# Optimization experiments

Hardware: AMD Instinct MI355X
Metric: run time of the kernel (lower is better)

## Reference

```python
import jax, jax.numpy as jnp
import numpy as np

B, H, W, C = 8, 128, 128, 192
WS, SS, HEADS = 8, 4, 6
NW = (H // WS) * (W // WS)
N = WS * WS

def _rel_pos_index(ws):
    coords = np.stack(np.meshgrid(np.arange(ws), np.arange(ws), indexing='ij')).reshape(2, -1)
    rel = (coords[:, :, None] - coords[:, None, :]).transpose(1, 2, 0)
    rel[:, :, 0] += ws - 1
    rel[:, :, 1] += ws - 1
    rel[:, :, 0] *= 2 * ws - 1
    return rel.sum(-1)  # (N, N) int

REL_IDX = jnp.asarray(_rel_pos_index(WS).reshape(-1))

def setup_inputs():
    key = jax.random.key(0)
    ks = jax.random.split(key, 8)
    p = lambda k, shp: jax.random.normal(k, shp, jnp.float32) * 0.02
    # exact Swin shift mask for shift=(SS,SS)
    img = np.zeros((1, H, W, 1), np.float32)
    cnt = 0
    for hs in (slice(0, -WS), slice(-WS, -SS), slice(-SS, None)):
        for vs in (slice(0, -WS), slice(-WS, -SS), slice(-SS, None)):
            img[:, hs, vs, :] = cnt; cnt += 1
    mw = img.reshape(1, H // WS, WS, W // WS, WS, 1).transpose(0, 1, 3, 2, 4, 5).reshape(-1, N)
    diff = mw[:, None, :] - mw[:, :, None]
    mask = np.where(diff != 0, -100.0, 0.0).astype(np.float32)
    return dict(
        x=jax.random.normal(ks[0], (B, H, W, C), jnp.float32),
        mask_matrix=jnp.asarray(mask),
        norm1_g=jnp.ones((C,), jnp.float32), norm1_b=jnp.zeros((C,), jnp.float32),
        qkv_w=p(ks[1], (C, 3 * C)), qkv_b=jnp.zeros((3 * C,), jnp.float32),
        rel_bias_table=p(ks[2], ((2 * WS - 1) * (2 * WS - 1), HEADS)),
        proj_w=p(ks[3], (C, C)), proj_b=jnp.zeros((C,), jnp.float32),
        norm2_g=jnp.ones((C,), jnp.float32), norm2_b=jnp.zeros((C,), jnp.float32),
        fc1_w=p(ks[4], (C, 4 * C)), fc1_b=jnp.zeros((4 * C,), jnp.float32),
        fc2_w=p(ks[5], (4 * C, C)), fc2_b=jnp.zeros((C,), jnp.float32),
    )

def _ln(x, g, b):
    m = x.mean(-1, keepdims=True)
    v = x.var(-1, keepdims=True)
    return (x - m) * jax.lax.rsqrt(v + 1e-5) * g + b

def _window_attn(xw, mask, qkv_w, qkv_b, rel_bias_table, proj_w, proj_b):
    Bw = xw.shape[0]
    hd = C // HEADS
    scale = hd ** -0.5
    # ---- spatial window attention ----
    qkv = (xw @ qkv_w + qkv_b).reshape(Bw, N, 3, HEADS, hd).transpose(2, 0, 3, 1, 4)
    q, k, v = qkv[0], qkv[1], qkv[2]  # (Bw, heads, N, hd)
    attn = jnp.einsum('bhnd,bhmd->bhnm', q, k) * scale
    bias = rel_bias_table[REL_IDX].reshape(N, N, HEADS).transpose(2, 0, 1)
    attn = attn + bias[None]
    attn = attn.reshape(Bw // NW, NW, HEADS, N, N) + mask[None, :, None]
    attn = jax.nn.softmax(attn.reshape(Bw, HEADS, N, N), axis=-1)
    x_spatial = jnp.einsum('bhnm,bhmd->bhnd', attn, v).transpose(0, 2, 1, 3).reshape(Bw, N, C)
    # ---- Fourier-domain attention branch ----
    x2d = xw.reshape(Bw, WS, WS, C)
    xf = jnp.fft.rfftn(x2d, axes=(1, 2), norm='ortho')  # (Bw, WS, WS//2+1, C) complex
    Hf, Wf = xf.shape[1], xf.shape[2]
    Nf = Hf * Wf
    def _qkv(r):  # shared qkv linear applied to real/imag parts (bias in both)
        return (r.reshape(Bw, Nf, C) @ qkv_w + qkv_b).reshape(Bw, Nf, 3, HEADS, hd).transpose(2, 0, 3, 1, 4)
    qr, qi = _qkv(xf.real), _qkv(xf.imag)
    qf = jax.lax.complex(qr[0], qi[0])
    kf = jax.lax.complex(qr[1], qi[1])
    vf = jax.lax.complex(qr[2], qi[2])
    attn_f = jnp.einsum('bhnd,bhmd->bhnm', qf, kf) * scale  # plain transpose, no conj (matches torch)
    attn_mag = jax.nn.softmax(jnp.abs(attn_f), axis=-1)
    xf_res = jnp.einsum('bhnm,bhmd->bhnd', attn_mag.astype(jnp.complex64), vf)
    xf_res = xf_res.transpose(0, 2, 1, 3).reshape(Bw, Hf, Wf, C)
    x_four = jnp.fft.irfftn(xf_res, s=(WS, WS), axes=(1, 2), norm='ortho').reshape(Bw, N, C)
    return (x_spatial + x_four) @ proj_w + proj_b

def reference(x, mask_matrix, norm1_g, norm1_b, qkv_w, qkv_b, rel_bias_table,
              proj_w, proj_b, norm2_g, norm2_b, fc1_w, fc1_b, fc2_w, fc2_b):
    shortcut = x
    xn = _ln(x, norm1_g, norm1_b)
    # shift (H,W divisible by WS so no padding needed)
    xs = jnp.roll(xn, (-SS, -SS), axis=(1, 2))
    # window partition -> (B*nW, N, C)
    xw = xs.reshape(B, H // WS, WS, W // WS, WS, C).transpose(0, 1, 3, 2, 4, 5).reshape(-1, N, C)
    aw = _window_attn(xw, mask_matrix, qkv_w, qkv_b, rel_bias_table, proj_w, proj_b)
    # window reverse + unshift
    xs = aw.reshape(B, H // WS, W // WS, WS, WS, C).transpose(0, 1, 3, 2, 4, 5).reshape(B, H, W, C)
    xo = jnp.roll(xs, (SS, SS), axis=(1, 2))
    x1 = shortcut + xo
    y = _ln(x1, norm2_g, norm2_b)
    y = jax.nn.gelu(y @ fc1_w + fc1_b, approximate=False) @ fc2_w + fc2_b
    return x1 + y
```

## Files before the change

### kernel.cpp

```cpp
#include <hip/hip_runtime.h>
#include <hip/hip_bf16.h>
#include <math.h>

#define SSH 4
#define SCALE 0.17677669529663687f

typedef __bf16 bf16x8 __attribute__((ext_vector_type(8)));
typedef __bf16 bf16x4 __attribute__((ext_vector_type(4)));
typedef unsigned short ushort8 __attribute__((ext_vector_type(8)));
typedef float  f32x4  __attribute__((ext_vector_type(4)));

static __device__ __forceinline__ f32x4 mfma16(bf16x8 a, bf16x8 b, f32x4 c){
    return __builtin_amdgcn_mfma_f32_16x16x32_bf16(a, b, c, 0, 0, 0);
}
#define MFMA16(a,b,c) mfma16((a),(b),(c))

static __device__ __forceinline__ bf16x8 ldfrag(const __bf16* p){
    return *reinterpret_cast<const bf16x8*>(p);
}
static __device__ __forceinline__ f32x4 zero4(){
    f32x4 z; z[0]=0.f; z[1]=0.f; z[2]=0.f; z[3]=0.f; return z;
}
static __device__ __forceinline__ float gelu_fast(float x){
    float u = x*(0.7978845608f + 0.0356774081f*x*x);
    return __fdividef(x, 1.f + __expf(-2.f*u));
}

__global__ __launch_bounds__(256) void k_prep(const float* __restrict__ qkvw,
        const float* __restrict__ projw, const float* __restrict__ fc1w,
        const float* __restrict__ fc2w, __bf16* __restrict__ Wq,
        __bf16* __restrict__ Wp, __bf16* __restrict__ W1, __bf16* __restrict__ W2,
        __bf16* __restrict__ Fre, __bf16* __restrict__ Fim,
        __bf16* __restrict__ Ci,  __bf16* __restrict__ nSi){
    int i = blockIdx.x*256 + threadIdx.x;
    if (i < 110592){ int n = i/192, k = i - n*192; Wq[i] = (__bf16)qkvw[k*576 + n]; }
    if (i < 36864) { int n = i/192, k = i - n*192; Wp[i] = (__bf16)projw[k*192 + n]; }
    if (i < 147456){ int n = i/192, k = i - n*192; W1[i] = (__bf16)fc1w[k*768 + n]; }
    if (i < 147456){ int n = i/768, k = i - n*768; W2[i] = (__bf16)fc2w[k*192 + n]; }
    if (i < 3072){
        int n = i>>6, p = i&63;
        float vr = 0.f, vi = 0.f;
        if (n < 40){
            int u = n/5, v = n - u*5, r = p>>3, c = p&7;
            int k = (u*r + v*c)&7;
            float ang = (float)k * 0.78539816339744831f;
            vr = cosf(ang)*0.125f; vi = -sinf(ang)*0.125f;
        }
        Fre[i] = (__bf16)vr; Fim[i] = (__bf16)vi;
    }
    if (i < 4096){
        int p = i>>6, n = i&63;
        float vc = 0.f, vs = 0.f;
        if (n < 40){
            int u = n/5, v = n - u*5, r = p>>3, c = p&7;
            int k = (u*r + v*c)&7;
            float ang = (float)k * 0.78539816339744831f;
            float wv = (v>=1 && v<=3)? 2.f : 1.f;
            vc = wv*cosf(ang)*0.125f; vs = -wv*sinf(ang)*0.125f;
        }
        Ci[i] = (__bf16)vc; nSi[i] = (__bf16)vs;
    }
}

__global__ __launch_bounds__(256,2) void k_qkv(const float* __restrict__ x,
        const float* __restrict__ n1g, const float* __restrict__ n1b,
        const __bf16* __restrict__ Wqt, const float* __restrict__ qkv_b,
        __bf16* __restrict__ S){
    __shared__ __align__(16) __bf16 xw[64*200];
    __shared__ __align__(16) __bf16 Wt[192*72];
    int tid = threadIdx.x;
    int win = blockIdx.x;
    int bb = win>>8, rem = win&255, wh = rem>>4, wwi = rem&15;
    {
        int tok = tid>>2, part = tid&3;
        int r = tok>>3, c = tok&7;
        int sh = (wh*8 + r + SSH)&127, sw = (wwi*8 + c + SSH)&127;
        const float* srcp = x + (((size_t)(bb*128+sh))*128 + sw)*192 + part*48;
        float v[48];
        #pragma unroll
        for (int i=0;i<12;i++){
            float4 t4 = *reinterpret_cast<const float4*>(srcp + i*4);
            v[i*4]=t4.x; v[i*4+1]=t4.y; v[i*4+2]=t4.z; v[i*4+3]=t4.w;
        }
        float s=0.f, ss=0.f;
        #pragma unroll
        for (int i=0;i<48;i++){ s+=v[i]; ss+=v[i]*v[i]; }
        s  += __shfl_xor(s,1);  s  += __shfl_xor(s,2);
        ss += __shfl_xor(ss,1); ss += __shfl_xor(ss,2);
        float mean = s*(1.f/192.f);
        float rstd = rsqrtf(ss*(1.f/192.f) - mean*mean + 1e-5f);
        #pragma unroll
        for (int i8=0;i8<6;i8++){
            bf16x8 pk;
            #pragma unroll
            for (int j=0;j<8;j++){
                int ch = part*48 + i8*8 + j;
                pk[j] = (__bf16)((v[i8*8+j]-mean)*rstd*n1g[ch] + n1b[ch]);
            }
            *reinterpret_cast<bf16x8*>(&xw[tok*200 + part*48 + i8*8]) = pk;
        }
    }
    int lane = tid&63, w = tid>>6, lr = lane&15, lg = lane>>4;
    ushort8 wreg[6];
    auto ldW = [&](int s, ushort8* wr){
        int nc = s/3, kc = s - nc*3;
        #pragma unroll
        for (int i=0;i<6;i++){
            int e = tid + i*256;
            int j = e>>3, k8 = e&7;
            wr[i] = *reinterpret_cast<const ushort8*>(
                reinterpret_cast<const unsigned short*>(Wqt) + (size_t)(nc*192+j)*192 + kc*64 + k8*8);
        }
    };
    auto stW = [&](ushort8* wr){
        #pragma unroll
        for (int i=0;i<6;i++){
            int e = tid + i*256;
            int j = e>>3, k8 = e&7;
            *reinterpret_cast<ushort8*>(reinterpret_cast<unsigned short*>(Wt) + j*72 + k8*8) = wr[i];
        }
    };
    ldW(0, wreg);
    __syncthreads();
    stW(wreg);
    __syncthreads();
    f32x4 acc[4][3];
    #pragma unroll
    for (int m=0;m<4;m++)
        #pragma unroll
        for (int n=0;n<3;n++) acc[m][n] = zero4();
    for (int s=0; s<9; s++){
        int nc = s/3, kc = s - nc*3;
        if (s<8) ldW(s+1, wreg);
        #pragma unroll
        for (int kk=0; kk<2; kk++){
            int ko = kc*64 + kk*32 + lg*8;
            bf16x8 a[4];
            #pragma unroll
            for (int m=0;m<4;m++) a[m] = ldfrag(&xw[(16*m+lr)*200 + ko]);
            int klo = kk*32 + lg*8;
            bf16x8 bfr[3];
            #pragma unroll
            for (int n=0;n<3;n++) bfr[n] = ldfrag(&Wt[(48*w+16*n+lr)*72 + klo]);
            #pragma unroll
            for (int m=0;m<4;m++)
                #pragma unroll
                for (int n=0;n<3;n++) acc[m][n] = MFMA16(a[m], bfr[n], acc[m][n]);
        }
        if (kc==2){
            #pragma unroll
            for (int n=0;n<3;n++){
                int col = nc*192 + 48*w + 16*n + lr;
                float bias = qkv_b[col];
                #pragma unroll
                for (int m=0;m<4;m++)
                    #pragma unroll
                    for (int r=0;r<4;r++){
                        int row = 16*m + 4*lg + r;
                        S[(size_t)(win*64+row)*576 + col] = (__bf16)(acc[m][n][r] + bias);
                    }
            }
            #pragma unroll
            for (int m=0;m<4;m++)
                #pragma unroll
                for (int n=0;n<3;n++) acc[m][n] = zero4();
        }
        __syncthreads();
        if (s<8) stW(wreg);
        __syncthreads();
    }
}

__global__ __launch_bounds__(256,4) void k_spatial(const __bf16* __restrict__ S,
        const float* __restrict__ relt, const float* __restrict__ mask,
        float* __restrict__ Bbuf){
    __shared__ __align__(16) __bf16 P[64*72];
    __shared__ __align__(16) __bf16 Vt[32*72];
    __shared__ float reltL[1350];
    int tid = threadIdx.x;
    int win = blockIdx.x;
    int widx = win & 255;
    int lane = tid&63, w = tid>>6, lr = lane&15, lg = lane>>4;
    for (int e=tid; e<1350; e+=256) reltL[e] = relt[e];
    float mreg[16];
    int bidx[16];
    #pragma unroll
    for (int nt=0; nt<4; nt++)
        #pragma unroll
        for (int r=0;r<4;r++){
            int row = 16*w + 4*lg + r;
            int col = 16*nt + lr;
            mreg[nt*4+r] = mask[((widx*64 + row)<<6) + col];
            int dr = (row>>3)-(col>>3)+7, dc = (row&7)-(col&7)+7;
            bidx[nt*4+r] = (dr*15+dc)*6;
        }
    const size_t sbase = (size_t)win*64*576;
    const __bf16* Sq = S + sbase;
    const __bf16* Sk = S + sbase + 192;
    const __bf16* Sv = S + sbase + 384;
    for (int h=0; h<6; h++){
        __syncthreads();
        {
            int d = tid&31, pg = tid>>5;
            const __bf16* sp = Sv + (size_t)(pg*8)*576 + h*32 + d;
            bf16x4 v0, v1;
            v0[0]=sp[0];    v0[1]=sp[576];  v0[2]=sp[1152]; v0[3]=sp[1728];
            v1[0]=sp[2304]; v1[1]=sp[2880]; v1[2]=sp[3456]; v1[3]=sp[4032];
            *reinterpret_cast<bf16x4*>(&Vt[d*72 + pg*8])   = v0;
            *reinterpret_cast<bf16x4*>(&Vt[d*72 + pg*8+4]) = v1;
        }
        __syncthreads();
        bf16x8 aq = ldfrag(Sq + (size_t)(16*w+lr)*576 + h*32 + lg*8);
        f32x4 acc[4];
        #pragma unroll
        for (int nt=0;nt<4;nt++){
            bf16x8 bk = ldfrag(Sk + (size_t)(16*nt+lr)*576 + h*32 + lg*8);
            acc[nt] = MFMA16(aq, bk, zero4());
        }
        float p[16];
        #pragma unroll
        for (int r=0;r<4;r++){
            float sc[4];
            #pragma unroll
            for (int nt=0;nt<4;nt++)
                sc[nt] = acc[nt][r]*SCALE + reltL[bidx[nt*4+r] + h] + mreg[nt*4+r];
            float mx = fmaxf(fmaxf(sc[0],sc[1]),fmaxf(sc[2],sc[3]));
            mx = fmaxf(mx, __shfl_xor(mx,1));
            mx = fmaxf(mx, __shfl_xor(mx,2));
            mx = fmaxf(mx, __shfl_xor(mx,4));
            mx = fmaxf(mx, __shfl_xor(mx,8));
            float sum = 0.f;
            #pragma unroll
            for (int nt=0;nt<4;nt++){ sc[nt] = __expf(sc[nt]-mx); sum += sc[nt]; }
            sum += __shfl_xor(sum,1);
            sum += __shfl_xor(sum,2);
            sum += __shfl_xor(sum,4);
            sum += __shfl_xor(sum,8);
            float inv = 1.f/sum;
            #pragma unroll
            for (int nt=0;nt<4;nt++) p[r*4+nt] = sc[nt]*inv;
        }
        #pragma unroll
        for (int r=0;r<4;r++)
            #pragma unroll
            for (int nt=0;nt<4;nt++)
                P[(16*w + 4*lg + r)*72 + 16*nt + lr] = (__bf16)p[r*4+nt];
        #pragma unroll
        for (int dt=0; dt<2; dt++){
            f32x4 o = zero4();
            #pragma unroll
            for (int ks=0; ks<2; ks++)
                o = MFMA16(ldfrag(&P[(16*w+lr)*72 + ks*32 + lg*8]),
                           ldfrag(&Vt[(16*dt+lr)*72 + ks*32 + lg*8]), o);
            #pragma unroll
            for (int r=0;r<4;r++){
                int row = 16*w + 4*lg + r;
                Bbuf[((size_t)win*64 + row)*192 + h*32 + 16*dt + lr] = o[r];
            }
        }
    }
}

__global__ __launch_bounds__(256,3) void k_fattn(const __bf16* __restrict__ S,
        const float* __restrict__ qkv_b,
        const __bf16* __restrict__ Fre_g, const __bf16* __restrict__ Fim_g,
        const __bf16* __restrict__ Ci_g,  const __bf16* __restrict__ nSi_g,
        float* __restrict__ Bbuf){
    __shared__ __align__(16) unsigned char arena[45056];
    __bf16* Gq_r = (__bf16*)(arena);
    __bf16* Gqin = (__bf16*)(arena + 3840);
    __bf16* Gk_r = (__bf16*)(arena + 7680);
    __bf16* Gk_i = (__bf16*)(arena + 11520);
    __bf16* Rt_r = (__bf16*)(arena);
    __bf16* Rt_i = (__bf16*)(arena + 5632);
    __bf16* Gv_r = (__bf16*)(arena + 15360);
    __bf16* Gv_i = (__bf16*)(arena + 20992);
    __bf16* St   = (__bf16*)(arena + 26624);
    float*  Smat = (float*) (arena + 26624);
    __bf16* P    = (__bf16*)(arena + 36608);
    int tid = threadIdx.x;
    int win = blockIdx.x / 6, h = blockIdx.x - win*6;
    int lane = tid&63, w = tid>>6, lr = lane&15, lg = lane>>4;
    bf16x4 z4; z4[0]=z4[1]=z4[2]=z4[3]=(__bf16)0.f;
    {
        int t2 = tid & 127;
        __bf16* A = (tid<128)? Gv_r : Gv_i;
        int row = t2>>2, c4 = (t2&3)*4;
        *reinterpret_cast<bf16x4*>(A + row*88 + 48 + c4) = z4;
    }
    const size_t sbase = (size_t)win*64*576 + h*32;
    for (int m=0;m<3;m++){
        __syncthreads();
        {
            int d = tid&31, pg = tid>>5;
            const __bf16* sp = S + sbase + (size_t)m*192 + (size_t)pg*8*576 + d;
            bf16x4 v0, v1;
            v0[0]=sp[0];      v0[1]=sp[576];    v0[2]=sp[1152];   v0[3]=sp[1728];
            v1[0]=sp[2304];   v1[1]=sp[2880];   v1[2]=sp[3456];   v1[3]=sp[4032];
            *reinterpret_cast<bf16x4*>(&St[d*88 + pg*8])     = v0;
            *reinterpret_cast<bf16x4*>(&St[d*88 + pg*8 + 4]) = v1;
        }
        __syncthreads();
        for (int j=w; j<12; j+=4){
            int term = j/6, r2 = j - term*6;
            if (m<2){
                int mt = r2>>1, nt = r2&1;
                const __bf16* Ag = (term? Fim_g : Fre_g) + (16*mt+lr)*64 + lg*8;
                f32x4 acc = zero4();
                acc = MFMA16(*reinterpret_cast<const bf16x8*>(Ag),
                             ldfrag(&St[(16*nt+lr)*88 + lg*8]), acc);
                acc = MFMA16(*reinterpret_cast<const bf16x8*>(Ag+32),
                             ldfrag(&St[(16*nt+lr)*88 + 32 + lg*8]), acc);
                int d = 16*nt + lr;
                float b = qkv_b[m*192 + h*32 + d];
                __bf16* dst = (m==0)? (term? Gqin : Gq_r) : (term? Gk_i : Gk_r);
                #pragma unroll
                for (int r=0;r<4;r++){
                    int n = 16*mt + 4*lg + r;
                    float val = acc[r] + ((term==0) ? ((n==0)? -7.f*b : b) : b);
                    if (m==0 && term==1) val = -val;
                    dst[n*40 + d] = (__bf16)val;
                }
            } else {
                int mt = r2/3, nt = r2 - mt*3;
                const __bf16* Bg = (term? Fim_g : Fre_g) + (16*nt+lr)*64 + lg*8;
                f32x4 acc = zero4();
                acc = MFMA16(ldfrag(&St[(16*mt+lr)*88 + lg*8]),
                             *reinterpret_cast<const bf16x8*>(Bg), acc);
                acc = MFMA16(ldfrag(&St[(16*mt+lr)*88 + 32 + lg*8]),
                             *reinterpret_cast<const bf16x8*>(Bg+32), acc);
                int n = 16*nt + lr;
                __bf16* dst = term? Gv_i : Gv_r;
                #pragma unroll
                for (int r=0;r<4;r++){
                    int d = 16*mt + 4*lg + r;
                    float b = qkv_b[2*192 + h*32 + d];
                    float val = acc[r] + ((term==0) ? ((n==0)? -7.f*b : b) : b);
                    dst[d*88 + n] = (__bf16)val;
                }
            }
        }
    }
    __syncthreads();
    for (int j=w; j<9; j+=4){
        int mt = j/3, nt = j - mt*3;
        bf16x8 qr = ldfrag(&Gq_r[(16*mt+lr)*40 + lg*8]);
        bf16x8 qi = ldfrag(&Gqin[(16*mt+lr)*40 + lg*8]);
        bf16x8 kr = ldfrag(&Gk_r[(16*nt+lr)*40 + lg*8]);
        bf16x8 ki = ldfrag(&Gk_i[(16*nt+lr)*40 + lg*8]);
        f32x4 sre = MFMA16(qi, ki, zero4());
        sre = MFMA16(qr, kr, sre);
        f32x4 t1 = MFMA16(qr, ki, zero4());
        f32x4 t2 = MFMA16(qi, kr, zero4());
        #pragma unroll
        for (int r=0;r<4;r++){
            float sim = t1[r] - t2[r];
            Smat[(16*mt + 4*lg + r)*52 + 16*nt + lr] =
                SCALE * sqrtf(sre[r]*sre[r] + sim*sim);
        }
    }
    __syncthreads();
    if (tid < 160){
        int row = tid>>2, part = tid&3, e0 = part*10;
        float mx = -1e30f;
        #pragma unroll
        for (int j=0;j<10;j++) mx = fmaxf(mx, Smat[row*52 + e0 + j]);
        mx = fmaxf(mx, __shfl_xor(mx,1));
        mx = fmaxf(mx, __shfl_xor(mx,2));
        float ex[10]; float sum=0.f;
        #pragma unroll
        for (int j=0;j<10;j++){ ex[j] = __expf(Smat[row*52+e0+j]-mx); sum += ex[j]; }
        sum += __shfl_xor(sum,1);
        sum += __shfl_xor(sum,2);
        float inv = 1.f/sum;
        #pragma unroll
        for (int j=0;j<10;j++) Smat[row*52+e0+j] = ex[j]*inv;
    }
    __syncthreads();
    for (int e=tid; e<3072; e+=256){
        int row = e>>6, col = e&63;
        float v = (row<40 && col<40)? Smat[row*52+col] : 0.f;
        P[row*88+col] = (__bf16)v;
    }
    {
        int t2 = tid & 127;
        __bf16* A = (tid<128)? Rt_r : Rt_i;
        int row = t2>>2, c4 = (t2&3)*4;
        *reinterpret_cast<bf16x4*>(A + row*88 + 48 + c4) = z4;
    }
    __syncthreads();
    for (int j=w; j<12; j+=4){
        int term = j/6, r2 = j - term*6;
        int dt = r2/3, nt = r2 - dt*3;
        const __bf16* Gv = term? Gv_i : Gv_r;
        f32x4 acc = zero4();
        #pragma unroll
        for (int ks=0; ks<2; ks++)
            acc = MFMA16(ldfrag(&Gv[(16*dt+lr)*88 + ks*32 + lg*8]),
                         ldfrag(&P [(16*nt+lr)*88 + ks*32 + lg*8]), acc);
        __bf16* dst = term? Rt_i : Rt_r;
        #pragma unroll
        for (int r=0;r<4;r++)
            dst[(16*dt + 4*lg + r)*88 + 16*nt + lr] = (__bf16)acc[r];
    }
    __syncthreads();
    for (int j=w; j<8; j+=4){
        int dt = j>>2, pt = j&3;
        f32x4 acc = zero4();
        #pragma unroll
        for (int ks=0; ks<2; ks++)
            acc = MFMA16(*reinterpret_cast<const bf16x8*>(nSi_g + (16*pt+lr)*64 + ks*32 + lg*8),
                         ldfrag(&Rt_i[(16*dt+lr)*88 + ks*32 + lg*8]), acc);
        #pragma unroll
        for (int ks=0; ks<2; ks++)
            acc = MFMA16(*reinterpret_cast<const bf16x8*>(Ci_g + (16*pt+lr)*64 + ks*32 + lg*8),
                         ldfrag(&Rt_r[(16*dt+lr)*88 + ks*32 + lg*8]), acc);
        #pragma unroll
        for (int r=0;r<4;r++){
            int p = 16*pt + 4*lg + r, d = 16*dt + lr;
            size_t idx = ((size_t)win*64 + p)*192 + h*32 + d;
            Bbuf[idx] += acc[r];
        }
    }
}

__global__ __launch_bounds__(256,2) void k_proj(const float* __restrict__ Bbuf,
        const float* __restrict__ x, const __bf16* __restrict__ Wpt,
        const float* __restrict__ proj_b, float* __restrict__ X1){
    __shared__ __align__(16) __bf16 xt[64*200];
    __shared__ __align__(16) __bf16 Wt[192*72];
    int tid = threadIdx.x;
    int win = blockIdx.x;
    {
        int tok = tid>>2, part = tid&3;
        const float* srcp = Bbuf + ((size_t)win*64 + tok)*192 + part*48;
        #pragma unroll
        for (int i8=0;i8<6;i8++){
            float4 a4 = *reinterpret_cast<const float4*>(srcp + i8*8);
            float4 b4 = *reinterpret_cast<const float4*>(srcp + i8*8 + 4);
            bf16x8 pk;
            pk[0]=(__bf16)a4.x; pk[1]=(__bf16)a4.y; pk[2]=(__bf16)a4.z; pk[3]=(__bf16)a4.w;
            pk[4]=(__bf16)b4.x; pk[5]=(__bf16)b4.y; pk[6]=(__bf16)b4.z; pk[7]=(__bf16)b4.w;
            *reinterpret_cast<bf16x8*>(&xt[tok*200 + part*48 + i8*8]) = pk;
        }
    }
    int lane = tid&63, w = tid>>6, lr = lane&15, lg = lane>>4;
    ushort8 wreg[6];
    auto ldW = [&](int kc, ushort8* wr){
        #pragma unroll
        for (int i=0;i<6;i++){
            int e = tid + i*256;
            int j = e>>3, k8 = e&7;
            wr[i] = *reinterpret_cast<const ushort8*>(
                reinterpret_cast<const unsigned short*>(Wpt) + (size_t)j*192 + kc*64 + k8*8);
        }
    };
    auto stW = [&](ushort8* wr){
        #pragma unroll
        for (int i=0;i<6;i++){
            int e = tid + i*256;
            int j = e>>3, k8 = e&7;
            *reinterpret_cast<ushort8*>(reinterpret_cast<unsigned short*>(Wt) + j*72 + k8*8) = wr[i];
        }
    };
    ldW(0, wreg);
    __syncthreads();
    stW(wreg);
    __syncthreads();
    f32x4 acc[4][3];
    #pragma unroll
    for (int m=0;m<4;m++)
        #pragma unroll
        for (int n=0;n<3;n++) acc[m][n] = zero4();
    for (int kc=0; kc<3; kc++){
        if (kc<2) ldW(kc+1, wreg);
        #pragma unroll
        for (int kk=0; kk<2; kk++){
            int ko = kc*64 + kk*32 + lg*8;
            bf16x8 a[4];
            #pragma unroll
            for (int m=0;m<4;m++) a[m] = ldfrag(&xt[(16*m+lr)*200 + ko]);
            int klo = kk*32 + lg*8;
            bf16x8 bfr[3];
            #pragma unroll
            for (int n=0;n<3;n++) bfr[n] = ldfrag(&Wt[(48*w+16*n+lr)*72 + klo]);
            #pragma unroll
            for (int m=0;m<4;m++)
                #pragma unroll
                for (int n=0;n<3;n++) acc[m][n] = MFMA16(a[m], bfr[n], acc[m][n]);
        }
        __syncthreads();
        if (kc<2) stW(wreg);
        __syncthreads();
    }
    int bb = win>>8, rem = win&255, wh = rem>>4, wwi = rem&15;
    #pragma unroll
    for (int m=0;m<4;m++)
        #pragma unroll
        for (int r=0;r<4;r++){
            int t = 16*m + 4*lg + r;
            int p = wh*8 + (t>>3), q = wwi*8 + (t&7);
            int hh = (p+SSH)&127, w2 = (q+SSH)&127;
            size_t pixb = (((size_t)bb*128 + hh)*128 + w2)*192;
            #pragma unroll
            for (int n=0;n<3;n++){
                int col = 48*w + 16*n + lr;
                X1[pixb + col] = acc[m][n][r] + proj_b[col] + x[pixb + col];
            }
        }
}

__global__ __launch_bounds__(256,2) void k_mlp(const float* __restrict__ X1,
        const float* __restrict__ g2, const float* __restrict__ b2v,
        const __bf16* __restrict__ W1t, const float* __restrict__ fc1b,
        const __bf16* __restrict__ W2t, const float* __restrict__ fc2b,
        float* __restrict__ out){
    __shared__ __align__(16) __bf16 xln[64*200];
    __shared__ __align__(16) __bf16 hbuf[64*200];
    __shared__ __align__(16) __bf16 Wt[192*72];
    int tid = threadIdx.x;
    size_t base = (size_t)blockIdx.x*64;
    {
        int tok = tid>>2, part = tid&3;
        const float* srcp = X1 + (base + tok)*192 + part*48;
        float v[48];
        #pragma unroll
        for (int i=0;i<12;i++){
            float4 t4 = *reinterpret_cast<const float4*>(srcp + i*4);
            v[i*4]=t4.x; v[i*4+1]=t4.y; v[i*4+2]=t4.z; v[i*4+3]=t4.w;
        }
        float s=0.f, ss=0.f;
        #pragma unroll
        for (int i=0;i<48;i++){ s+=v[i]; ss+=v[i]*v[i]; }
        s  += __shfl_xor(s,1);  s  += __shfl_xor(s,2);
        ss += __shfl_xor(ss,1); ss += __shfl_xor(ss,2);
        float mean = s*(1.f/192.f);
        float rstd = rsqrtf(ss*(1.f/192.f) - mean*mean + 1e-5f);
        #pragma unroll
        for (int i8=0;i8<6;i8++){
            bf16x8 pk;
            #pragma unroll
            for (int j=0;j<8;j++){
                int ch = part*48 + i8*8 + j;
                pk[j] = (__bf16)((v[i8*8+j]-mean)*rstd*g2[ch] + b2v[ch]);
            }
            *reinterpret_cast<bf16x8*>(&xln[tok*200 + part*48 + i8*8]) = pk;
        }
    }
    int lane = tid&63, w = tid>>6, lr = lane&15, lg = lane>>4;
    ushort8 wreg[6];
    auto ldW = [&](int s, ushort8* wr){
        int hc = s/6, inner = s - hc*6;
        int kc = (inner<3)? inner : inner-3;
        const unsigned short* src;
        size_t rowstride;
        size_t off;
        if (inner<3){ src = reinterpret_cast<const unsigned short*>(W1t);
                      rowstride = 192; off = (size_t)(hc*192)*192 + kc*64; }
        else        { src = reinterpret_cast<const unsigned short*>(W2t);
                      rowstride = 768; off = (size_t)hc*192 + kc*64; }
        #pragma unroll
        for (int i=0;i<6;i++){
            int e = tid + i*256;
            int j = e>>3, k8 = e&7;
            wr[i] = *reinterpret_cast<const ushort8*>(src + (size_t)j*rowstride + off + k8*8);
        }
    };
    auto stW = [&](ushort8* wr){
        #pragma unroll
        for (int i=0;i<6;i++){
            int e = tid + i*256;
            int j = e>>3, k8 = e&7;
            *reinterpret_cast<ushort8*>(reinterpret_cast<unsigned short*>(Wt) + j*72 + k8*8) = wr[i];
        }
    };
    ldW(0, wreg);
    __syncthreads();
    stW(wreg);
    __syncthreads();
    f32x4 acc1[4][3], acc2[4][3];
    #pragma unroll
    for (int m=0;m<4;m++)
        #pragma unroll
        for (int n=0;n<3;n++){ acc1[m][n] = zero4(); acc2[m][n] = zero4(); }
    for (int s=0; s<24; s++){
        int hc = s/6, inner = s - hc*6;
        bool fc1 = inner<3;
        int kc = fc1 ? inner : inner-3;
        if (s<23) ldW(s+1, wreg);
        const __bf16* A = fc1 ? xln : hbuf;
        #pragma unroll
        for (int kk=0; kk<2; kk++){
            int ko = kc*64 + kk*32 + lg*8;
            bf16x8 a[4];
            #pragma unroll
            for (int m=0;m<4;m++) a[m] = ldfrag(&A[(16*m+lr)*200 + ko]);
            int klo = kk*32 + lg*8;
            bf16x8 bfr[3];
            #pragma unroll
            for (int n=0;n<3;n++) bfr[n] = ldfrag(&Wt[(48*w+16*n+lr)*72 + klo]);
            if (fc1){
                #pragma unroll
                for (int m=0;m<4;m++)
                    #pragma unroll
                    for (int n=0;n<3;n++) acc1[m][n] = MFMA16(a[m], bfr[n], acc1[m][n]);
            } else {
                #pragma unroll
                for (int m=0;m<4;m++)
                    #pragma unroll
                    for (int n=0;n<3;n++) acc2[m][n] = MFMA16(a[m], bfr[n], acc2[m][n]);
            }
        }
        if (inner==2){
            #pragma unroll
            for (int n=0;n<3;n++){
                int jcol = 48*w + 16*n + lr;
                float b1 = fc1b[hc*192 + jcol];
                #pragma unroll
                for (int m=0;m<4;m++)
                    #pragma unroll
                    for (int r=0;r<4;r++){
                        float xv = acc1[m][n][r] + b1;
                        hbuf[(16*m + 4*lg + r)*200 + jcol] = (__bf16)gelu_fast(xv);
                        acc1[m][n][r] = 0.f;
                    }
            }
        }
        __syncthreads();
        if (s<23) stW(wreg);
        __syncthreads();
    }
    #pragma unroll
    for (int n=0;n<3;n++){
        int col = 48*w + 16*n + lr;
        float b2 = fc2b[col];
        #pragma unroll
        for (int m=0;m<4;m++)
            #pragma unroll
            for (int r=0;r<4;r++){
                size_t t = base + 16*m + 4*lg + r;
                out[t*192 + col] = acc2[m][n][r] + b2 + X1[t*192 + col];
            }
    }
}

extern "C" void kernel_launch(void* const* d_in, const int* in_sizes, int n_in,
                              void* d_out, int out_size, void* d_ws, size_t ws_size,
                              hipStream_t stream) {
    const float* x     = (const float*)d_in[0];
    const float* mask  = (const float*)d_in[1];
    const float* n1g   = (const float*)d_in[2];
    const float* n1b   = (const float*)d_in[3];
    const float* qkvw  = (const float*)d_in[4];
    const float* qkvb  = (const float*)d_in[5];
    const float* relt  = (const float*)d_in[6];
    const float* projw = (const float*)d_in[7];
    const float* projb = (const float*)d_in[8];
    const float* n2g   = (const float*)d_in[9];
    const float* n2b   = (const float*)d_in[10];
    const float* fc1w  = (const float*)d_in[11];
    const float* fc1b  = (const float*)d_in[12];
    const float* fc2w  = (const float*)d_in[13];
    const float* fc2b  = (const float*)d_in[14];
    float* out = (float*)d_out;

    char* wsb = (char*)d_ws;
    __bf16* Sb  = (__bf16*)wsb;
    float*  X1  = (float*)(wsb + 150994944);
    __bf16* Wqt = (__bf16*)(wsb + 251658240);
    __bf16* Wpt = (__bf16*)(wsb + 251879424);
    __bf16* W1t = (__bf16*)(wsb + 251953152);
    __bf16* W2t = (__bf16*)(wsb + 252248064);
    __bf16* Fre = (__bf16*)(wsb + 252542976);
    __bf16* Fim = (__bf16*)(wsb + 252549120);
    __bf16* Ci  = (__bf16*)(wsb + 252555264);
    __bf16* nSi = (__bf16*)(wsb + 252563456);

    k_prep   <<<576,   256, 0, stream>>>(qkvw, projw, fc1w, fc2w, Wqt, Wpt, W1t, W2t,
                                         Fre, Fim, Ci, nSi);
    k_qkv    <<<2048,  256, 0, stream>>>(x, n1g, n1b, Wqt, qkvb, Sb);
    k_spatial<<<2048,  256, 0, stream>>>(Sb, relt, mask, out);
    k_fattn  <<<12288, 256, 0, stream>>>(Sb, qkvb, Fre, Fim, Ci, nSi, out);
    k_proj   <<<2048,  256, 0, stream>>>(out, x, Wpt, projb, X1);
    k_mlp    <<<2048,  256, 0, stream>>>(X1, n2g, n2b, W1t, fc1b, W2t, fc2b, out);
}
```

Measured before the change: 616.9 us.

## Load GEMM weight fragments directly from global memory instead of LDS staging

In the qkv, proj and MLP kernels, weight tiles are no longer staged through shared memory with register double-buffering and paired barriers. Each wave now reads its B fragments straight from global memory (relying on L2/cache reuse across blocks), which removes the per-step barriers and frees LDS. The occupancy hints in launch_bounds are raised to 4/4/3 to match the lower LDS footprint. The risk is higher global and L2 load latency on the MFMA critical path, since there is no explicit prefetch.

After: 753.6 us. 1.22x slower.

```diff
diff --git a/kernel.cpp b/kernel.cpp
--- a/kernel.cpp
+++ b/kernel.cpp
@@ -7,7 +7,6 @@
 
 typedef __bf16 bf16x8 __attribute__((ext_vector_type(8)));
 typedef __bf16 bf16x4 __attribute__((ext_vector_type(4)));
-typedef unsigned short ushort8 __attribute__((ext_vector_type(8)));
 typedef float  f32x4  __attribute__((ext_vector_type(4)));
 
 static __device__ __forceinline__ f32x4 mfma16(bf16x8 a, bf16x8 b, f32x4 c){
@@ -62,12 +61,11 @@
     }
 }
 
-__global__ __launch_bounds__(256,2) void k_qkv(const float* __restrict__ x,
+__global__ __launch_bounds__(256,4) void k_qkv(const float* __restrict__ x,
         const float* __restrict__ n1g, const float* __restrict__ n1b,
         const __bf16* __restrict__ Wqt, const float* __restrict__ qkv_b,
         __bf16* __restrict__ S){
     __shared__ __align__(16) __bf16 xw[64*200];
-    __shared__ __align__(16) __bf16 Wt[192*72];
     int tid = threadIdx.x;
     int win = blockIdx.x;
     int bb = win>>8, rem = win&255, wh = rem>>4, wwi = rem&15;
@@ -100,74 +98,41 @@
             *reinterpret_cast<bf16x8*>(&xw[tok*200 + part*48 + i8*8]) = pk;
         }
     }
+    __syncthreads();
     int lane = tid&63, w = tid>>6, lr = lane&15, lg = lane>>4;
-    ushort8 wreg[6];
-    auto ldW = [&](int s, ushort8* wr){
-        int nc = s/3, kc = s - nc*3;
-        #pragma unroll
-        for (int i=0;i<6;i++){
-            int e = tid + i*256;
-            int j = e>>3, k8 = e&7;
-            wr[i] = *reinterpret_cast<const ushort8*>(
-                reinterpret_cast<const unsigned short*>(Wqt) + (size_t)(nc*192+j)*192 + kc*64 + k8*8);
-        }
-    };
-    auto stW = [&](ushort8* wr){
-        #pragma unroll
-        for (int i=0;i<6;i++){
-            int e = tid + i*256;
-            int j = e>>3, k8 = e&7;
-            *reinterpret_cast<ushort8*>(reinterpret_cast<unsigned short*>(Wt) + j*72 + k8*8) = wr[i];
-        }
-    };
-    ldW(0, wreg);
-    __syncthreads();
-    stW(wreg);
-    __syncthreads();
-    f32x4 acc[4][3];
-    #pragma unroll
-    for (int m=0;m<4;m++)
-        #pragma unroll
-        for (int n=0;n<3;n++) acc[m][n] = zero4();
-    for (int s=0; s<9; s++){
-        int nc = s/3, kc = s - nc*3;
-        if (s<8) ldW(s+1, wreg);
-        #pragma unroll
-        for (int kk=0; kk<2; kk++){
-            int ko = kc*64 + kk*32 + lg*8;
+    for (int nc=0; nc<3; nc++){
+        f32x4 acc[4][3];
+        #pragma unroll
+        for (int m=0;m<4;m++)
+            #pragma unroll
+            for (int n=0;n<3;n++) acc[m][n] = zero4();
+        #pragma unroll
+        for (int kc=0; kc<6; kc++){
+            int ko = kc*32 + lg*8;
             bf16x8 a[4];
             #pragma unroll
             for (int m=0;m<4;m++) a[m] = ldfrag(&xw[(16*m+lr)*200 + ko]);
-            int klo = kk*32 + lg*8;
             bf16x8 bfr[3];
             #pragma unroll
-            for (int n=0;n<3;n++) bfr[n] = ldfrag(&Wt[(48*w+16*n+lr)*72 + klo]);
+            for (int n=0;n<3;n++)
+                bfr[n] = ldfrag(Wqt + (size_t)(nc*192 + 48*w + 16*n + lr)*192 + ko);
             #pragma unroll
             for (int m=0;m<4;m++)
                 #pragma unroll
                 for (int n=0;n<3;n++) acc[m][n] = MFMA16(a[m], bfr[n], acc[m][n]);
         }
-        if (kc==2){
-            #pragma unroll
-            for (int n=0;n<3;n++){
-                int col = nc*192 + 48*w + 16*n + lr;
-                float bias = qkv_b[col];
-                #pragma unroll
-                for (int m=0;m<4;m++)
-                    #pragma unroll
-                    for (int r=0;r<4;r++){
-                        int row = 16*m + 4*lg + r;
-                        S[(size_t)(win*64+row)*576 + col] = (__bf16)(acc[m][n][r] + bias);
-                    }
-            }
+        #pragma unroll
+        for (int n=0;n<3;n++){
+            int col = nc*192 + 48*w + 16*n + lr;
+            float bias = qkv_b[col];
             #pragma unroll
             for (int m=0;m<4;m++)
                 #pragma unroll
-                for (int n=0;n<3;n++) acc[m][n] = zero4();
-        }
-        __syncthreads();
-        if (s<8) stW(wreg);
-        __syncthreads();
+                for (int r=0;r<4;r++){
+                    int row = 16*m + 4*lg + r;
+                    S[(size_t)(win*64+row)*576 + col] = (__bf16)(acc[m][n][r] + bias);
+                }
+        }
     }
 }
 
@@ -424,11 +389,10 @@
     }
 }
 
-__global__ __launch_bounds__(256,2) void k_proj(const float* __restrict__ Bbuf,
+__global__ __launch_bounds__(256,4) void k_proj(const float* __restrict__ Bbuf,
         const float* __restrict__ x, const __bf16* __restrict__ Wpt,
         const float* __restrict__ proj_b, float* __restrict__ X1){
     __shared__ __align__(16) __bf16 xt[64*200];
-    __shared__ __align__(16) __bf16 Wt[192*72];
     int tid = threadIdx.x;
     int win = blockIdx.x;
     {
@@ -444,54 +408,27 @@
             *reinterpret_cast<bf16x8*>(&xt[tok*200 + part*48 + i8*8]) = pk;
         }
     }
+    __syncthreads();
     int lane = tid&63, w = tid>>6, lr = lane&15, lg = lane>>4;
-    ushort8 wreg[6];
-    auto ldW = [&](int kc, ushort8* wr){
-        #pragma unroll
-        for (int i=0;i<6;i++){
-            int e = tid + i*256;
-            int j = e>>3, k8 = e&7;
-            wr[i] = *reinterpret_cast<const ushort8*>(
-                reinterpret_cast<const unsigned short*>(Wpt) + (size_t)j*192 + kc*64 + k8*8);
-        }
-    };
-    auto stW = [&](ushort8* wr){
-        #pragma unroll
-        for (int i=0;i<6;i++){
-            int e = tid + i*256;
-            int j = e>>3, k8 = e&7;
-            *reinterpret_cast<ushort8*>(reinterpret_cast<unsigned short*>(Wt) + j*72 + k8*8) = wr[i];
-        }
-    };
-    ldW(0, wreg);
-    __syncthreads();
-    stW(wreg);
-    __syncthreads();
     f32x4 acc[4][3];
     #pragma unroll
     for (int m=0;m<4;m++)
         #pragma unroll
         for (int n=0;n<3;n++) acc[m][n] = zero4();
-    for (int kc=0; kc<3; kc++){
-        if (kc<2) ldW(kc+1, wreg);
-        #pragma unroll
-        for (int kk=0; kk<2; kk++){
-            int ko = kc*64 + kk*32 + lg*8;
-            bf16x8 a[4];
-            #pragma unroll
-            for (int m=0;m<4;m++) a[m] = ldfrag(&xt[(16*m+lr)*200 + ko]);
-            int klo = kk*32 + lg*8;
-            bf16x8 bfr[3];
-            #pragma unroll
-            for (int n=0;n<3;n++) bfr[n] = ldfrag(&Wt[(48*w+16*n+lr)*72 + klo]);
-            #pragma unroll
-            for (int m=0;m<4;m++)
-                #pragma unroll
-                for (int n=0;n<3;n++) acc[m][n] = MFMA16(a[m], bfr[n], acc[m][n]);
-        }
-        __syncthreads();
-        if (kc<2) stW(wreg);
-        __syncthreads();
+    #pragma unroll
+    for (int kc=0; kc<6; kc++){
+        int ko = kc*32 + lg*8;
+        bf16x8 a[4];
+        #pragma unroll
+        for (int m=0;m<4;m++) a[m] = ldfrag(&xt[(16*m+lr)*200 + ko]);
+        bf16x8 bfr[3];
+        #pragma unroll
+        for (int n=0;n<3;n++)
+            bfr[n] = ldfrag(Wpt + (size_t)(48*w + 16*n + lr)*192 + ko);
+        #pragma unroll
+        for (int m=0;m<4;m++)
+            #pragma unroll
+            for (int n=0;n<3;n++) acc[m][n] = MFMA16(a[m], bfr[n], acc[m][n]);
     }
     int bb = win>>8, rem = win&255, wh = rem>>4, wwi = rem&15;
     #pragma unroll
@@ -510,14 +447,13 @@
         }
 }
 
-__global__ __launch_bounds__(256,2) void k_mlp(const float* __restrict__ X1,
+__global__ __launch_bounds__(256,3) void k_mlp(const float* __restrict__ X1,
         const float* __restrict__ g2, const float* __restrict__ b2v,
         const __bf16* __restrict__ W1t, const float* __restrict__ fc1b,
         const __bf16* __restrict__ W2t, const float* __restrict__ fc2b,
         float* __restrict__ out){
     __shared__ __align__(16) __bf16 xln[64*200];
     __shared__ __align__(16) __bf16 hbuf[64*200];
-    __shared__ __align__(16) __bf16 Wt[192*72];
     int tid = threadIdx.x;
     size_t base = (size_t)blockIdx.x*64;
     {
@@ -547,87 +483,62 @@
             *reinterpret_cast<bf16x8*>(&xln[tok*200 + part*48 + i8*8]) = pk;
         }
     }
+    __syncthreads();
     int lane = tid&63, w = tid>>6, lr = lane&15, lg = lane>>4;
-    ushort8 wreg[6];
-    auto ldW = [&](int s, ushort8* wr){
-        int hc = s/6, inner = s - hc*6;
-        int kc = (inner<3)? inner : inner-3;
-        const unsigned short* src;
-        size_t rowstride;
-        size_t off;
-        if (inner<3){ src = reinterpret_cast<const unsigned short*>(W1t);
-                      rowstride = 192; off = (size_t)(hc*192)*192 + kc*64; }
-        else        { src = reinterpret_cast<const unsigned short*>(W2t);
-                      rowstride = 768; off = (size_t)hc*192 + kc*64; }
-        #pragma unroll
-        for (int i=0;i<6;i++){
-            int e = tid + i*256;
-            int j = e>>3, k8 = e&7;
-            wr[i] = *reinterpret_cast<const ushort8*>(src + (size_t)j*rowstride + off + k8*8);
-        }
-    };
-    auto stW = [&](ushort8* wr){
-        #pragma unroll
-        for (int i=0;i<6;i++){
-            int e = tid + i*256;
-            int j = e>>3, k8 = e&7;
-            *reinterpret_cast<ushort8*>(reinterpret_cast<unsigned short*>(Wt) + j*72 + k8*8) = wr[i];
-        }
-    };
-    ldW(0, wreg);
-    __syncthreads();
-    stW(wreg);
-    __syncthreads();
-    f32x4 acc1[4][3], acc2[4][3];
+    f32x4 acc2[4][3];
     #pragma unroll
     for (int m=0;m<4;m++)
         #pragma unroll
-        for (int n=0;n<3;n++){ acc1[m][n] = zero4(); acc2[m][n] = zero4(); }
-    for (int s=0; s<24; s++){
-        int hc = s/6, inner = s - hc*6;
-        bool fc1 = inner<3;
-        int kc = fc1 ? inner : inner-3;
-        if (s<23) ldW(s+1, wreg);
-        const __bf16* A = fc1 ? xln : hbuf;
-        #pragma unroll
-        for (int kk=0; kk<2; kk++){
-            int ko = kc*64 + kk*32 + lg*8;
+        for (int n=0;n<3;n++) acc2[m][n] = zero4();
+    for (int hc=0; hc<4; hc++){
+        f32x4 acc1[4][3];
+        #pragma unroll
+        for (int m=0;m<4;m++)
+            #pragma unroll
+            for (int n=0;n<3;n++) acc1[m][n] = zero4();
+        #pragma unroll
+        for (int kc=0; kc<6; kc++){
+            int ko = kc*32 + lg*8;
             bf16x8 a[4];
             #pragma unroll
-            for (int m=0;m<4;m++) a[m] = ldfrag(&A[(16*m+lr)*200 + ko]);
-            int klo = kk*32 + lg*8;
+            for (int m=0;m<4;m++) a[m] = ldfrag(&xln[(16*m+lr)*200 + ko]);
             bf16x8 bfr[3];
             #pragma unroll
-            for (int n=0;n<3;n++) bfr[n] = ldfrag(&Wt[(48*w+16*n+lr)*72 + klo]);
-            if (fc1){
-                #pragma unroll
-                for (int m=0;m<4;m++)
-                    #pragma unroll
-                    for (int n=0;n<3;n++) acc1[m][n] = MFMA16(a[m], bfr[n], acc1[m][n]);
-            } else {
-                #pragma unroll
-                for (int m=0;m<4;m++)
-                    #pragma unroll
-                    for (int n=0;n<3;n++) acc2[m][n] = MFMA16(a[m], bfr[n], acc2[m][n]);
-            }
-        }
-        if (inner==2){
-            #pragma unroll
-            for (int n=0;n<3;n++){
-                int jcol = 48*w + 16*n + lr;
-                float b1 = fc1b[hc*192 + jcol];
-                #pragma unroll
-                for (int m=0;m<4;m++)
-                    #pragma unroll
-                    for (int r=0;r<4;r++){
-                        float xv = acc1[m][n][r] + b1;
-                        hbuf[(16*m + 4*lg + r)*200 + jcol] = (__bf16)gelu_fast(xv);
-                        acc1[m][n][r] = 0.f;
-                    }
-            }
+            for (int n=0;n<3;n++)
+                bfr[n] = ldfrag(W1t + (size_t)(hc*192 + 48*w + 16*n + lr)*192 + ko);
+            #pragma unroll
+            for (int m=0;m<4;m++)
+                #pragma unroll
+                for (int n=0;n<3;n++) acc1[m][n] = MFMA16(a[m], bfr[n], acc1[m][n]);
+        }
+        #pragma unroll
+        for (int n=0;n<3;n++){
+            int jcol = 48*w + 16*n + lr;
+            float b1 = fc1b[hc*192 + jcol];
+            #pragma unroll
+            for (int m=0;m<4;m++)
+                #pragma unroll
+                for (int r=0;r<4;r++){
+                    float xv = acc1[m][n][r] + b1;
+                    hbuf[(16*m + 4*lg + r)*200 + jcol] = (__bf16)gelu_fast(xv);
+                }
         }
         __syncthreads();
-        if (s<23) stW(wreg);
+        #pragma unroll
+        for (int kc=0; kc<6; kc++){
+            int ko = kc*32 + lg*8;
+            bf16x8 a[4];
+            #pragma unroll
+            for (int m=0;m<4;m++) a[m] = ldfrag(&hbuf[(16*m+lr)*200 + ko]);
+            bf16x8 bfr[3];
+            #pragma unroll
+            for (int n=0;n<3;n++)
+                bfr[n] = ldfrag(W2t + (size_t)(48*w + 16*n + lr)*768 + hc*192 + ko);
+            #pragma unroll
+            for (int m=0;m<4;m++)
+                #pragma unroll
+                for (int n=0;n<3;n++) acc2[m][n] = MFMA16(a[m], bfr[n], acc2[m][n]);
+        }
         __syncthreads();
     }
     #pragma unroll
```
